# Kernel optimization log

Hardware: AMD Instinct MI355X
Metric: run time of the kernel (lower is better)

The kernel has to match this reference:

```python
import jax, jax.numpy as jnp
import numpy as np

N, E, D, H = 8192, 262144, 128, 64


def setup_inputs() -> dict:
    key = jax.random.key(0)
    ks = jax.random.split(key, 6)
    edge_index = jax.random.randint(ks[0], (2, E), 0, N, dtype=jnp.int64)
    adj = jnp.zeros((N, N), jnp.float32).at[edge_index[0], edge_index[1]].set(1.0)
    embed = jax.random.normal(ks[1], (N, D), jnp.float32)
    noise = jax.random.uniform(ks[2], (E,), jnp.float32, minval=1e-6, maxval=1.0 - 1e-6)
    W1 = jax.random.normal(ks[3], (2 * D, H), jnp.float32) / np.float32(np.sqrt(2 * D))
    b1 = jnp.zeros((H,), jnp.float32)
    W2 = jax.random.normal(ks[4], (H, 1), jnp.float32) / np.float32(np.sqrt(H))
    b2 = jnp.zeros((1,), jnp.float32)
    return {"embed": embed, "adj": adj, "noise": noise, "W1": W1, "b1": b1,
            "W2": W2, "b2": b2, "edge_index": edge_index}


def reference(embed, adj, noise, W1, b1, W2, b2, edge_index):
    row, col = edge_index[0], edge_index[1]
    # edge gather + concat: [E, 2D]
    h = jnp.concatenate([embed[row], embed[col]], axis=-1)
    # elayers: Linear(2D,64) -> ReLU -> Linear(64,1)
    log_alpha = (jax.nn.relu(h @ W1 + b1) @ W2 + b2).reshape(-1)  # [E]
    # concrete sigmoid sampling, beta (tmp) = 1.0
    gate = jax.nn.sigmoid(jnp.log(noise) - jnp.log1p(-noise) + log_alpha)
    # sparse COO build + coalesce (sum duplicates) + to_dense
    n = adj.shape[0]
    mask = jnp.zeros((n, n), adj.dtype).at[row, col].add(gate)
    # symmetrize and apply adjacency
    sym = 0.5 * (mask + mask.T)
    masked_adj = adj * sym
    return masked_adj
```

## Files before the change

### kernel.cpp

```cpp
#include <hip/hip_runtime.h>
#include <hip/hip_bf16.h>

#define NN 8192
#define EE 262144
#define DD 128
#define HH 64

#define PRE_BLOCKS  2048
#define FILL_BLOCKS 8192
#define EPW 16

__global__ void init_kernel(const float* __restrict__ embed,
                            const float* __restrict__ W1,
                            float* __restrict__ Pt,
                            float* __restrict__ Pb,
                            float4* __restrict__ out4) {
    const int tid = threadIdx.x;
    const int b   = blockIdx.x;

    if (b >= PRE_BLOCKS) {
        const size_t base = (size_t)(b - PRE_BLOCKS) * 2048 + tid;
        const float4 z = make_float4(0.f, 0.f, 0.f, 0.f);
#pragma unroll
        for (int i = 0; i < 8; ++i)
            out4[base + (size_t)i * 256] = z;
        return;
    }

    const int w    = tid >> 6;
    const int lane = tid & 63;
    const int n    = (b << 2) + w;

    __shared__ float esh[4][DD];
    esh[w][lane]      = embed[n * DD + lane];
    esh[w][lane + 64] = embed[n * DD + 64 + lane];
    __syncthreads();

    float at = 0.f, ab = 0.f;
#pragma unroll 8
    for (int k = 0; k < DD; ++k) {
        float ek = esh[w][k];
        at = fmaf(ek, W1[k * HH + lane],        at);
        ab = fmaf(ek, W1[(DD + k) * HH + lane], ab);
    }
    Pt[n * HH + lane] = at;
    Pb[n * HH + lane] = ab;
}

__global__ void edge_kernel(const float4* __restrict__ Pt4,
                            const float4* __restrict__ Pb4,
                            const float* __restrict__ b1,
                            const float* __restrict__ W2,
                            const float* __restrict__ b2,
                            const float* __restrict__ noise,
                            const int* __restrict__ ei,
                            const float* __restrict__ adj,
                            float* __restrict__ out) {
    const int tid  = threadIdx.x;
    const int lane = tid & 63;
    const int q    = lane & 15;
    const int g16  = lane >> 4;

    __shared__ int sflag;
    if (tid < 64) {
        int v = ei[2 * tid + 1];
        unsigned long long bal = __ballot(v != 0);
        if (tid == 0) sflag = (bal == 0ULL) ? 1 : 0;
    }
    __syncthreads();
    const bool i64 = (sflag != 0);

    const int wav   = (blockIdx.x << 2) + (tid >> 6);
    const int ebase = wav * EPW + g16 * 4;

    int r[4], c[4];
    if (i64) {
#pragma unroll
        for (int i = 0; i < 4; ++i) {
            r[i] = ei[2 * (ebase + i)];
            c[i] = ei[2 * (EE + ebase + i)];
        }
    } else {
#pragma unroll
        for (int i = 0; i < 4; ++i) {
            r[i] = ei[ebase + i];
            c[i] = ei[EE + ebase + i];
        }
    }

    const float4 bb = ((const float4*)b1)[q];
    const float4 ww = ((const float4*)W2)[q];

    float v[4];
#pragma unroll
    for (int i = 0; i < 4; ++i) {
        const float4 pt = Pt4[r[i] * 16 + q];
        const float4 pb = Pb4[c[i] * 16 + q];
        v[i] = fmaxf(pt.x + pb.x + bb.x, 0.f) * ww.x
             + fmaxf(pt.y + pb.y + bb.y, 0.f) * ww.y
             + fmaxf(pt.z + pb.z + bb.z, 0.f) * ww.z
             + fmaxf(pt.w + pb.w + bb.w, 0.f) * ww.w;
    }

#pragma unroll
    for (int i = 0; i < 4; ++i)
#pragma unroll
        for (int off = 8; off; off >>= 1)
            v[i] += __shfl_xor(v[i], off, 64);

    if (q == 0) {
        const float bias2 = b2[0];
        float u[4], a[4];
#pragma unroll
        for (int i = 0; i < 4; ++i) {
            u[i] = noise[ebase + i];
            a[i] = adj[(size_t)c[i] * NN + r[i]];
        }
#pragma unroll
        for (int i = 0; i < 4; ++i) {
            const float la    = v[i] + bias2;
            const float logit = logf(u[i]) - log1pf(-u[i]) + la;
            const float g2    = 0.5f / (1.f + expf(-logit));
            atomicAdd(&out[(size_t)r[i] * NN + c[i]], g2);
            if (a[i] != 0.f)
                atomicAdd(&out[(size_t)c[i] * NN + r[i]], g2 * a[i]);
        }
    }
}

extern "C" void kernel_launch(void* const* d_in, const int* in_sizes, int n_in,
                              void* d_out, int out_size, void* d_ws, size_t ws_size,
                              hipStream_t stream) {
    const float* embed = (const float*)d_in[0];
    const float* adj   = (const float*)d_in[1];
    const float* noise = (const float*)d_in[2];
    const float* W1    = (const float*)d_in[3];
    const float* b1    = (const float*)d_in[4];
    const float* W2    = (const float*)d_in[5];
    const float* b2    = (const float*)d_in[6];
    const int*   ei    = (const int*)d_in[7];
    float* out = (float*)d_out;

    float* Pt = (float*)d_ws;
    float* Pb = Pt + (size_t)NN * HH;

    init_kernel<<<PRE_BLOCKS + FILL_BLOCKS, 256, 0, stream>>>(
        embed, W1, Pt, Pb, (float4*)out);
    edge_kernel<<<EE / (EPW * 4), 256, 0, stream>>>(
        (const float4*)Pt, (const float4*)Pb, b1, W2, b2, noise, ei, adj, out);
}
```

Baseline: 448.7 us.

## Split edge gate computation from scatter and overlap gate with output zero-fill

Restructures the pipeline into three kernels. The precompute runs alone. Gate computation is fused with the 256MB output zero-fill so the MLP gather work overlaps the memory-bound fill. A separate one-edge-per-thread scatter kernel then does the adj lookup and the atomics. This moves the latency-bound random adj reads and atomics out of the MLP kernel and gives them full-thread parallelism. The cost is an extra launch and a round trip of the gate values through workspace memory.

```diff
diff --git a/kernel.cpp b/kernel.cpp
--- a/kernel.cpp
+++ b/kernel.cpp
@@ -6,30 +6,18 @@
 #define DD 128
 #define HH 64
 
-#define PRE_BLOCKS  2048
+#define GATE_BLOCKS (EE / 64)
 #define FILL_BLOCKS 8192
-#define EPW 16
+#define SCAT_BLOCKS (EE / 256)
 
-__global__ void init_kernel(const float* __restrict__ embed,
-                            const float* __restrict__ W1,
-                            float* __restrict__ Pt,
-                            float* __restrict__ Pb,
-                            float4* __restrict__ out4) {
-    const int tid = threadIdx.x;
-    const int b   = blockIdx.x;
-
-    if (b >= PRE_BLOCKS) {
-        const size_t base = (size_t)(b - PRE_BLOCKS) * 2048 + tid;
-        const float4 z = make_float4(0.f, 0.f, 0.f, 0.f);
-#pragma unroll
-        for (int i = 0; i < 8; ++i)
-            out4[base + (size_t)i * 256] = z;
-        return;
-    }
-
+__global__ void precompute_kernel(const float* __restrict__ embed,
+                                  const float* __restrict__ W1,
+                                  float* __restrict__ Pt,
+                                  float* __restrict__ Pb) {
+    const int tid  = threadIdx.x;
     const int w    = tid >> 6;
     const int lane = tid & 63;
-    const int n    = (b << 2) + w;
+    const int n    = (blockIdx.x << 2) + w;
 
     __shared__ float esh[4][DD];
     esh[w][lane]      = embed[n * DD + lane];
@@ -47,16 +35,26 @@
     Pb[n * HH + lane] = ab;
 }
 
-__global__ void edge_kernel(const float4* __restrict__ Pt4,
-                            const float4* __restrict__ Pb4,
-                            const float* __restrict__ b1,
-                            const float* __restrict__ W2,
-                            const float* __restrict__ b2,
-                            const float* __restrict__ noise,
-                            const int* __restrict__ ei,
-                            const float* __restrict__ adj,
-                            float* __restrict__ out) {
-    const int tid  = threadIdx.x;
+__global__ void fill_gate_kernel(const float4* __restrict__ Pt4,
+                                 const float4* __restrict__ Pb4,
+                                 const float* __restrict__ b1,
+                                 const float* __restrict__ W2,
+                                 const float* __restrict__ b2,
+                                 const float* __restrict__ noise,
+                                 const int* __restrict__ ei,
+                                 float* __restrict__ g2out,
+                                 float4* __restrict__ out4) {
+    const int tid = threadIdx.x;
+
+    if (blockIdx.x >= GATE_BLOCKS) {
+        const size_t base = (size_t)(blockIdx.x - GATE_BLOCKS) * 2048 + tid;
+        const float4 z = make_float4(0.f, 0.f, 0.f, 0.f);
+#pragma unroll
+        for (int i = 0; i < 8; ++i)
+            out4[base + (size_t)i * 256] = z;
+        return;
+    }
+
     const int lane = tid & 63;
     const int q    = lane & 15;
     const int g16  = lane >> 4;
@@ -70,8 +68,7 @@
     __syncthreads();
     const bool i64 = (sflag != 0);
 
-    const int wav   = (blockIdx.x << 2) + (tid >> 6);
-    const int ebase = wav * EPW + g16 * 4;
+    const int ebase = (blockIdx.x << 6) + ((tid >> 6) << 4) + (g16 << 2);
 
     int r[4], c[4];
     if (i64) {
@@ -110,22 +107,44 @@
 
     if (q == 0) {
         const float bias2 = b2[0];
-        float u[4], a[4];
 #pragma unroll
         for (int i = 0; i < 4; ++i) {
-            u[i] = noise[ebase + i];
-            a[i] = adj[(size_t)c[i] * NN + r[i]];
-        }
-#pragma unroll
-        for (int i = 0; i < 4; ++i) {
-            const float la    = v[i] + bias2;
-            const float logit = logf(u[i]) - log1pf(-u[i]) + la;
-            const float g2    = 0.5f / (1.f + expf(-logit));
-            atomicAdd(&out[(size_t)r[i] * NN + c[i]], g2);
-            if (a[i] != 0.f)
-                atomicAdd(&out[(size_t)c[i] * NN + r[i]], g2 * a[i]);
+            const float u     = noise[ebase + i];
+            const float logit = logf(u) - log1pf(-u) + v[i] + bias2;
+            g2out[ebase + i]  = 0.5f / (1.f + expf(-logit));
         }
     }
+}
+
+__global__ void scatter_kernel(const float* __restrict__ g2in,
+                               const int* __restrict__ ei,
+                               const float* __restrict__ adj,
+                               float* __restrict__ out) {
+    const int tid = threadIdx.x;
+
+    __shared__ int sflag;
+    if (tid < 64) {
+        int v = ei[2 * tid + 1];
+        unsigned long long bal = __ballot(v != 0);
+        if (tid == 0) sflag = (bal == 0ULL) ? 1 : 0;
+    }
+    __syncthreads();
+
+    const int e = (blockIdx.x << 8) + tid;
+    int r, c;
+    if (sflag) {
+        r = ei[2 * e];
+        c = ei[2 * (EE + e)];
+    } else {
+        r = ei[e];
+        c = ei[EE + e];
+    }
+
+    const float g2 = g2in[e];
+    const float a  = adj[(size_t)c * NN + r];
+    atomicAdd(&out[(size_t)r * NN + c], g2);
+    if (a != 0.f)
+        atomicAdd(&out[(size_t)c * NN + r], g2 * a);
 }
 
 extern "C" void kernel_launch(void* const* d_in, const int* in_sizes, int n_in,
@@ -143,9 +162,11 @@
 
     float* Pt = (float*)d_ws;
     float* Pb = Pt + (size_t)NN * HH;
+    float* g2 = Pb + (size_t)NN * HH;
 
-    init_kernel<<<PRE_BLOCKS + FILL_BLOCKS, 256, 0, stream>>>(
-        embed, W1, Pt, Pb, (float4*)out);
-    edge_kernel<<<EE / (EPW * 4), 256, 0, stream>>>(
-        (const float4*)Pt, (const float4*)Pb, b1, W2, b2, noise, ei, adj, out);
+    precompute_kernel<<<NN / 4, 256, 0, stream>>>(embed, W1, Pt, Pb);
+    fill_gate_kernel<<<GATE_BLOCKS + FILL_BLOCKS, 256, 0, stream>>>(
+        (const float4*)Pt, (const float4*)Pb, b1, W2, b2, noise, ei, g2,
+        (float4*)out);
+    scatter_kernel<<<SCAT_BLOCKS, 256, 0, stream>>>(g2, ei, adj, out);
 }
```

After: 453.4 us. No clear change (+1.0%).

## Fuse projection, zero-fill and edge scatter into one cooperative persistent kernel

Applied to the files above, without the earlier changes.

Merges the per-node projection/zero-fill kernel and the edge kernel into a single cooperative launch of 1024 blocks, separated by a grid-wide sync. The 256 MB output zero-fill now uses nontemporal vector stores. Edge indices and noise are loaded as int4/float4 vectors, and the concrete-sigmoid gate is rewritten algebraically as u/(u+(1-u)e^{-la}) with fast exp, which avoids the log and log1p calls. The aim is to drop one launch and its boundary, at the cost of grid-sync overhead and fewer, larger blocks doing the fill.

```diff
diff --git a/kernel.cpp b/kernel.cpp
--- a/kernel.cpp
+++ b/kernel.cpp
@@ -1,129 +1,139 @@
 #include <hip/hip_runtime.h>
 #include <hip/hip_bf16.h>
+#include <hip/hip_cooperative_groups.h>
+
+namespace cg = cooperative_groups;
 
 #define NN 8192
 #define EE 262144
 #define DD 128
 #define HH 64
+#define NB 1024
+#define NT 256
 
-#define PRE_BLOCKS  2048
-#define FILL_BLOCKS 8192
-#define EPW 16
+typedef float f32x4 __attribute__((ext_vector_type(4)));
 
-__global__ void init_kernel(const float* __restrict__ embed,
-                            const float* __restrict__ W1,
-                            float* __restrict__ Pt,
-                            float* __restrict__ Pb,
-                            float4* __restrict__ out4) {
-    const int tid = threadIdx.x;
-    const int b   = blockIdx.x;
-
-    if (b >= PRE_BLOCKS) {
-        const size_t base = (size_t)(b - PRE_BLOCKS) * 2048 + tid;
-        const float4 z = make_float4(0.f, 0.f, 0.f, 0.f);
-#pragma unroll
-        for (int i = 0; i < 8; ++i)
-            out4[base + (size_t)i * 256] = z;
-        return;
-    }
-
+__global__ void __launch_bounds__(NT, 4) fused_kernel(
+    const float* __restrict__ embed,
+    const float* __restrict__ adj,
+    const float* __restrict__ noise,
+    const float* __restrict__ W1,
+    const float* __restrict__ b1,
+    const float* __restrict__ W2,
+    const float* __restrict__ b2,
+    const int*   __restrict__ ei,
+    float* __restrict__ Pt,
+    float* __restrict__ Pb,
+    float* __restrict__ out)
+{
+    const int tid  = threadIdx.x;
+    const int b    = blockIdx.x;
     const int w    = tid >> 6;
     const int lane = tid & 63;
-    const int n    = (b << 2) + w;
 
     __shared__ float esh[4][DD];
-    esh[w][lane]      = embed[n * DD + lane];
-    esh[w][lane + 64] = embed[n * DD + 64 + lane];
-    __syncthreads();
+    __shared__ int   sflag;
 
-    float at = 0.f, ab = 0.f;
-#pragma unroll 8
-    for (int k = 0; k < DD; ++k) {
-        float ek = esh[w][k];
-        at = fmaf(ek, W1[k * HH + lane],        at);
-        ab = fmaf(ek, W1[(DD + k) * HH + lane], ab);
-    }
-    Pt[n * HH + lane] = at;
-    Pb[n * HH + lane] = ab;
-}
-
-__global__ void edge_kernel(const float4* __restrict__ Pt4,
-                            const float4* __restrict__ Pb4,
-                            const float* __restrict__ b1,
-                            const float* __restrict__ W2,
-                            const float* __restrict__ b2,
-                            const float* __restrict__ noise,
-                            const int* __restrict__ ei,
-                            const float* __restrict__ adj,
-                            float* __restrict__ out) {
-    const int tid  = threadIdx.x;
-    const int lane = tid & 63;
-    const int q    = lane & 15;
-    const int g16  = lane >> 4;
-
-    __shared__ int sflag;
     if (tid < 64) {
         int v = ei[2 * tid + 1];
         unsigned long long bal = __ballot(v != 0);
         if (tid == 0) sflag = (bal == 0ULL) ? 1 : 0;
     }
-    __syncthreads();
+
+#pragma unroll 1
+    for (int it = 0; it < 2; ++it) {
+        const int n = (b << 3) + (it << 2) + w;
+        __syncthreads();
+        esh[w][lane]      = embed[n * DD + lane];
+        esh[w][lane + 64] = embed[n * DD + 64 + lane];
+        __syncthreads();
+        float at = 0.f, ab = 0.f;
+#pragma unroll 8
+        for (int k = 0; k < DD; ++k) {
+            const float ek = esh[w][k];
+            at = fmaf(ek, W1[k * HH + lane],        at);
+            ab = fmaf(ek, W1[(DD + k) * HH + lane], ab);
+        }
+        Pt[n * HH + lane] = at;
+        Pb[n * HH + lane] = ab;
+    }
+
+    {
+        f32x4* out4 = (f32x4*)out;
+        const f32x4 z = {0.f, 0.f, 0.f, 0.f};
+        const size_t base = (size_t)b * (64 * NT) + tid;
+#pragma unroll
+        for (int i = 0; i < 64; ++i)
+            __builtin_nontemporal_store(z, &out4[base + (size_t)i * NT]);
+    }
+
+    cg::this_grid().sync();
+
     const bool i64 = (sflag != 0);
+    const int q    = lane & 15;
+    const int grp  = (w << 2) + (lane >> 4);
 
-    const int wav   = (blockIdx.x << 2) + (tid >> 6);
-    const int ebase = wav * EPW + g16 * 4;
+    const float4 bb    = ((const float4*)b1)[q];
+    const float4 ww    = ((const float4*)W2)[q];
+    const float  bias2 = b2[0];
+    const float4* Pt4  = (const float4*)Pt;
+    const float4* Pb4  = (const float4*)Pb;
 
-    int r[4], c[4];
-    if (i64) {
+#pragma unroll 1
+    for (int p = 0; p < 4; ++p) {
+        const int ebase = (b << 8) + (p << 6) + (grp << 2);
+
+        int r[4], c[4];
+        if (i64) {
+            const int4 r0 = ((const int4*)ei)[(ebase >> 1)];
+            const int4 r1 = ((const int4*)ei)[(ebase >> 1) + 1];
+            const int4 c0 = ((const int4*)(ei + 2 * EE))[(ebase >> 1)];
+            const int4 c1 = ((const int4*)(ei + 2 * EE))[(ebase >> 1) + 1];
+            r[0] = r0.x; r[1] = r0.z; r[2] = r1.x; r[3] = r1.z;
+            c[0] = c0.x; c[1] = c0.z; c[2] = c1.x; c[3] = c1.z;
+        } else {
+            const int4 rr = ((const int4*)ei)[ebase >> 2];
+            const int4 cc = ((const int4*)(ei + EE))[ebase >> 2];
+            r[0] = rr.x; r[1] = rr.y; r[2] = rr.z; r[3] = rr.w;
+            c[0] = cc.x; c[1] = cc.y; c[2] = cc.z; c[3] = cc.w;
+        }
+
+        float u[4], a[4];
+        if (q == 0) {
+            const float4 un = ((const float4*)noise)[ebase >> 2];
+            u[0] = un.x; u[1] = un.y; u[2] = un.z; u[3] = un.w;
+#pragma unroll
+            for (int i = 0; i < 4; ++i)
+                a[i] = adj[(size_t)c[i] * NN + r[i]];
+        }
+
+        float v[4];
 #pragma unroll
         for (int i = 0; i < 4; ++i) {
-            r[i] = ei[2 * (ebase + i)];
-            c[i] = ei[2 * (EE + ebase + i)];
+            const float4 pt = Pt4[r[i] * 16 + q];
+            const float4 pb = Pb4[c[i] * 16 + q];
+            v[i] = fmaxf(pt.x + pb.x + bb.x, 0.f) * ww.x
+                 + fmaxf(pt.y + pb.y + bb.y, 0.f) * ww.y
+                 + fmaxf(pt.z + pb.z + bb.z, 0.f) * ww.z
+                 + fmaxf(pt.w + pb.w + bb.w, 0.f) * ww.w;
         }
-    } else {
-#pragma unroll
-        for (int i = 0; i < 4; ++i) {
-            r[i] = ei[ebase + i];
-            c[i] = ei[EE + ebase + i];
-        }
-    }
-
-    const float4 bb = ((const float4*)b1)[q];
-    const float4 ww = ((const float4*)W2)[q];
-
-    float v[4];
-#pragma unroll
-    for (int i = 0; i < 4; ++i) {
-        const float4 pt = Pt4[r[i] * 16 + q];
-        const float4 pb = Pb4[c[i] * 16 + q];
-        v[i] = fmaxf(pt.x + pb.x + bb.x, 0.f) * ww.x
-             + fmaxf(pt.y + pb.y + bb.y, 0.f) * ww.y
-             + fmaxf(pt.z + pb.z + bb.z, 0.f) * ww.z
-             + fmaxf(pt.w + pb.w + bb.w, 0.f) * ww.w;
-    }
 
 #pragma unroll
-    for (int i = 0; i < 4; ++i)
+        for (int i = 0; i < 4; ++i)
 #pragma unroll
-        for (int off = 8; off; off >>= 1)
-            v[i] += __shfl_xor(v[i], off, 64);
+            for (int off = 8; off; off >>= 1)
+                v[i] += __shfl_xor(v[i], off, 64);
 
-    if (q == 0) {
-        const float bias2 = b2[0];
-        float u[4], a[4];
+        if (q == 0) {
 #pragma unroll
-        for (int i = 0; i < 4; ++i) {
-            u[i] = noise[ebase + i];
-            a[i] = adj[(size_t)c[i] * NN + r[i]];
-        }
-#pragma unroll
-        for (int i = 0; i < 4; ++i) {
-            const float la    = v[i] + bias2;
-            const float logit = logf(u[i]) - log1pf(-u[i]) + la;
-            const float g2    = 0.5f / (1.f + expf(-logit));
-            atomicAdd(&out[(size_t)r[i] * NN + c[i]], g2);
-            if (a[i] != 0.f)
-                atomicAdd(&out[(size_t)c[i] * NN + r[i]], g2 * a[i]);
+            for (int i = 0; i < 4; ++i) {
+                const float la = v[i] + bias2;
+                const float ex = __expf(-la);
+                const float g2 = 0.5f * u[i] / (u[i] + (1.f - u[i]) * ex);
+                atomicAdd(&out[(size_t)r[i] * NN + c[i]], g2);
+                if (a[i] != 0.f)
+                    atomicAdd(&out[(size_t)c[i] * NN + r[i]], g2 * a[i]);
+            }
         }
     }
 }
@@ -144,8 +154,9 @@
     float* Pt = (float*)d_ws;
     float* Pb = Pt + (size_t)NN * HH;
 
-    init_kernel<<<PRE_BLOCKS + FILL_BLOCKS, 256, 0, stream>>>(
-        embed, W1, Pt, Pb, (float4*)out);
-    edge_kernel<<<EE / (EPW * 4), 256, 0, stream>>>(
-        (const float4*)Pt, (const float4*)Pb, b1, W2, b2, noise, ei, adj, out);
+    void* args[] = {(void*)&embed, (void*)&adj, (void*)&noise, (void*)&W1,
+                    (void*)&b1, (void*)&W2, (void*)&b2, (void*)&ei,
+                    (void*)&Pt, (void*)&Pb, (void*)&out};
+    (void)hipLaunchCooperativeKernel(reinterpret_cast<void*>(fused_kernel),
+                                     dim3(NB), dim3(NT), args, 0, stream);
 }
```

Result: slower. 625.7 us (+39.4%).
